# Kernel tuning notes

Measured on AMD Instinct MI355X. Metric: run time of the kernel, lower is better.

## Reference

```python
import jax, jax.numpy as jnp
import numpy as np

HEAD_NUM = 16
MASK_FILL = 100000.0  # source uses +1e5 on masked entries (not -inf)


def setup_inputs() -> dict:
    key = jax.random.key(0)
    k1, k2, k3, k4, k5 = jax.random.split(key, 5)
    B, S, E = 2, 2048, 1024
    scale = 0.02
    return {
        "x": jax.random.normal(k1, (B, S, E), dtype=jnp.float32),
        "W_atten": jax.random.normal(k2, (E, 3 * E), dtype=jnp.float32) * scale,
        "b_atten": jax.random.normal(k3, (3 * E,), dtype=jnp.float32) * scale,
        "W_proj": jax.random.normal(k4, (E, E), dtype=jnp.float32) * scale,
        "b_proj": jax.random.normal(k5, (E,), dtype=jnp.float32) * scale,
    }


def reference(x, W_atten, b_atten, W_proj, b_proj):
    B, S, E = x.shape
    H = HEAD_NUM
    hd = E // H
    # QKV projection: [B, S, 3E]
    qkv = x @ W_atten + b_atten
    # reshape [B, S, H, 3*hd] -> [B, H, S, 3*hd], chunk into q,k,v [B,H,S,hd]
    qkv = jnp.transpose(qkv.reshape(B, S, H, 3 * hd), (0, 2, 1, 3))
    q, k, v = jnp.split(qkv, 3, axis=-1)
    # raw scores, NO 1/sqrt(dk) scaling (faithful to source)
    w = jnp.einsum("bhqd,bhkd->bhqk", q, k)
    # causal mask applied as w*mask + (1-mask)*1e5 (faithful to source)
    mask = jnp.tril(jnp.ones((S, S), dtype=w.dtype))
    w = w * mask + (1.0 - mask) * MASK_FILL
    # softmax over dim=1 == HEAD axis (faithful to source quirk)
    w = jax.nn.softmax(w, axis=1)
    # attn_drop: identity in eval mode
    a = jnp.einsum("bhqk,bhkd->bhqd", w, v)  # [B,H,S,hd]
    a = jnp.transpose(a, (0, 2, 1, 3)).reshape(B, S, E)
    h = a @ W_proj + b_proj
    # resi_drop: identity in eval mode
    return h
```

## Files before the change

kernel.cpp:

```cpp
#include <hip/hip_runtime.h>

#define DI __device__ __forceinline__

typedef __attribute__((ext_vector_type(8))) short s16x8;
typedef __attribute__((ext_vector_type(4))) short s16x4;
typedef __attribute__((ext_vector_type(4))) float f32x4;

DI unsigned short f2bf(float f){
  unsigned u = __float_as_uint(f);
  u = (u + 0x7FFFu + ((u >> 16) & 1u)) >> 16;
  return (unsigned short)u;
}
DI float bf2f(unsigned short h){
  return __uint_as_float(((unsigned)h) << 16);
}

DI void gll16(const void* g, void* l){
  __builtin_amdgcn_global_load_lds((const __attribute__((address_space(1))) void*)g,
                                   (__attribute__((address_space(3))) void*)l, 16, 0, 0);
}

__global__ void cvt_kernel(const float* __restrict__ in, unsigned short* __restrict__ out, int n8){
  int i = blockIdx.x * blockDim.x + threadIdx.x;
  if (i >= n8) return;
  const float4* p = (const float4*)in + (size_t)i * 2;
  float4 a = p[0], b = p[1];
  s16x8 o;
  o[0] = (short)f2bf(a.x); o[1] = (short)f2bf(a.y); o[2] = (short)f2bf(a.z); o[3] = (short)f2bf(a.w);
  o[4] = (short)f2bf(b.x); o[5] = (short)f2bf(b.y); o[6] = (short)f2bf(b.z); o[7] = (short)f2bf(b.w);
  ((s16x8*)out)[i] = o;
}

__global__ void transpose_cvt(const float* __restrict__ in, unsigned short* __restrict__ out, int R, int C){
  __shared__ float t[32][33];
  int c0 = blockIdx.x * 32, r0 = blockIdx.y * 32;
  int tx = threadIdx.x, ty = threadIdx.y;
  #pragma unroll
  for (int i = 0; i < 4; i++)
    t[ty + i*8][tx] = in[(size_t)(r0 + ty + i*8) * C + c0 + tx];
  __syncthreads();
  #pragma unroll
  for (int i = 0; i < 4; i++)
    out[(size_t)(c0 + ty + i*8) * R + r0 + tx] = f2bf(t[tx][ty + i*8]);
}

template<int MODE, int BM>
__launch_bounds__(256)
__global__ void gemm_kernel(const unsigned short* __restrict__ A,
                            const unsigned short* __restrict__ Wt,
                            const float* __restrict__ bias,
                            int N,
                            unsigned short* __restrict__ qb,
                            unsigned short* __restrict__ kb,
                            unsigned short* __restrict__ vt,
                            float* __restrict__ out)
{
  constexpr int MI = BM / 32;
  constexpr int AC = BM / 32;
  const int K = 1024;
  __shared__ unsigned short As[BM * 64];
  __shared__ unsigned short Bs[128 * 64];
  int m0 = blockIdx.y * BM, n0 = blockIdx.x * 128;
  int tid = threadIdx.x;
  int lane = tid & 63, w = tid >> 6;
  int row_l = lane & 15, kgrp = lane >> 4;
  int wm = (w >> 1) * (MI * 16), wn = (w & 1) * 64;

  const unsigned short* asrc[AC];
  const unsigned short* bsrc[4];
  int ldsoA[AC], ldsoB[4];
  int chunk = (lane & 7) ^ (lane >> 3);
  #pragma unroll
  for (int c4 = 0; c4 < AC; c4++){
    int r = c4*32 + w*8 + (lane >> 3);
    asrc[c4] = A + (size_t)(m0 + r) * K + chunk*8;
    ldsoA[c4] = (c4*32 + w*8) * 64;
  }
  #pragma unroll
  for (int c4 = 0; c4 < 4; c4++){
    int r = c4*32 + w*8 + (lane >> 3);
    bsrc[c4] = Wt + (size_t)(n0 + r) * K + chunk*8;
    ldsoB[c4] = (c4*32 + w*8) * 64;
  }
  int eA[MI], eB[4];
  #pragma unroll
  for (int i = 0; i < MI; i++){
    int ra = wm + i*16 + row_l;
    eA[i] = (ra*64 + kgrp*8) ^ ((ra & 7) << 3);
  }
  #pragma unroll
  for (int i = 0; i < 4; i++){
    int rb = wn + i*16 + row_l;
    eB[i] = (rb*64 + kgrp*8) ^ ((rb & 7) << 3);
  }

  f32x4 acc[MI][4];
  #pragma unroll
  for (int i = 0; i < MI; i++)
    #pragma unroll
    for (int j = 0; j < 4; j++)
      acc[i][j] = (f32x4){0.f, 0.f, 0.f, 0.f};

  for (int k0 = 0; k0 < K; k0 += 64){
    #pragma unroll
    for (int c4 = 0; c4 < AC; c4++)
      gll16(asrc[c4] + k0, (void*)(As + ldsoA[c4]));
    #pragma unroll
    for (int c4 = 0; c4 < 4; c4++)
      gll16(bsrc[c4] + k0, (void*)(Bs + ldsoB[c4]));
    __syncthreads();
    #pragma unroll
    for (int kc = 0; kc < 2; kc++){
      s16x8 af[MI], bfr[4];
      #pragma unroll
      for (int mi = 0; mi < MI; mi++)
        af[mi] = *(const s16x8*)&As[eA[mi] ^ (kc*32)];
      #pragma unroll
      for (int ni = 0; ni < 4; ni++)
        bfr[ni] = *(const s16x8*)&Bs[eB[ni] ^ (kc*32)];
      #pragma unroll
      for (int mi = 0; mi < MI; mi++)
        #pragma unroll
        for (int ni = 0; ni < 4; ni++)
          acc[mi][ni] = __builtin_amdgcn_mfma_f32_16x16x32_bf16(af[mi], bfr[ni], acc[mi][ni], 0, 0, 0);
    }
    __syncthreads();
  }

  #pragma unroll
  for (int mi = 0; mi < MI; mi++){
    #pragma unroll
    for (int ni = 0; ni < 4; ni++){
      #pragma unroll
      for (int j = 0; j < 4; j++){
        int gr = m0 + wm + mi*16 + kgrp*4 + j;
        int gc = n0 + wn + ni*16 + row_l;
        float v = acc[mi][ni][j] + bias[gc];
        if (MODE == 0){
          int h = gc / 192, cc = gc % 192;
          int b = gr >> 11, s = gr & 2047;
          unsigned short bv = f2bf(v);
          if (cc < 64){
            qb[(size_t)gr * 1024 + h*64 + cc] = bv;
          } else if (cc < 128){
            int d = cc - 64; int kt = s >> 6, kk = s & 63;
            kb[(size_t)((b*16 + h)*32 + kt) * 4096 + ((kk*64 + d) ^ ((kk & 7) << 3))] = bv;
          } else {
            int d = cc - 128; int kt = s >> 6, kk = s & 63;
            vt[(size_t)((b*16 + h)*32 + kt) * 4096 + ((d*64 + kk) ^ ((d & 7) << 3))] = bv;
          }
        } else {
          out[(size_t)gr * N + gc] = v;
        }
      }
    }
  }
}

__global__ void sufv_kernel(const unsigned short* __restrict__ vt, float* __restrict__ sufv){
  __shared__ float tot[4][64];
  int bh = blockIdx.x;
  int tid = threadIdx.x;
  int tq = tid >> 6, d = tid & 63;
  const unsigned short* base = vt + (size_t)bh * 32 * 4096;
  float s[8];
  float run = 0.f;
  for (int j = 7; j >= 0; j--){
    int t = tq*8 + j;
    float rs = 0.f;
    #pragma unroll
    for (int c = 0; c < 8; c++){
      int idx = (d*64 + c*8) ^ ((d & 7) << 3);
      s16x8 v = *(const s16x8*)&base[(size_t)t*4096 + idx];
      #pragma unroll
      for (int e = 0; e < 8; e++) rs += bf2f((unsigned short)v[e]);
    }
    run += rs; s[j] = run;
  }
  tot[tq][d] = run;
  __syncthreads();
  float carry = 0.f;
  for (int t2 = tq+1; t2 < 4; t2++) carry += tot[t2][d];
  #pragma unroll
  for (int j = 0; j < 8; j++)
    sufv[((size_t)bh*33 + tq*8 + j)*64 + d] = s[j] + carry;
  if (tid < 64) sufv[((size_t)bh*33 + 32)*64 + tid] = 0.f;
}

__launch_bounds__(256)
__global__ void dpass_kernel(const unsigned short* __restrict__ qbuf,
                             const unsigned short* __restrict__ kb,
                             float* __restrict__ invDQ)
{
  __shared__ unsigned short Kst[4][4096];
  int bid = blockIdx.x;
  int blk = (bid & 7) * 132 + (bid >> 3);
  int b = blk / 528, t = blk % 528;
  int kt = (int)(32.5f - sqrtf(1056.25f - 2.f*t));
  while (kt*(65-kt)/2 > t) kt--;
  while ((kt+1)*(64-kt)/2 <= t) kt++;
  int qt = kt + (t - kt*(65-kt)/2);

  int tid = threadIdx.x, lane = tid & 63, w = tid >> 6;
  int row_l = lane & 15, kgrp = lane >> 4;

  const unsigned short* ktb = kb + ((size_t)(b*16)*32 + kt) * 4096;
  int sgoff = (w*128 + lane)*8;

  auto stage = [&](int hh, int buf){
    const unsigned short* src = ktb + (size_t)hh * 131072;
    gll16(src + sgoff,       (void*)(&Kst[buf][0] + w*1024));
    gll16(src + sgoff + 512, (void*)(&Kst[buf][0] + w*1024 + 512));
  };

  int e0[4];
  #pragma unroll
  for (int ks = 0; ks < 4; ks++){
    int row = ks*16 + row_l;
    e0[ks] = (row*64 + kgrp*8) ^ ((row & 7) << 3);
  }

  stage(0, 0);
  stage(1, 1);

  f32x4 esum[4];
  #pragma unroll
  for (int ks = 0; ks < 4; ks++) esum[ks] = (f32x4){0.f,0.f,0.f,0.f};

  const unsigned short* qrow_p = qbuf + (size_t)(b*2048 + qt*64 + w*16 + row_l) * 1024;
  s16x8 qf0 = *(const s16x8*)&qrow_p[kgrp*8];
  s16x8 qf1 = *(const s16x8*)&qrow_p[32 + kgrp*8];

  for (int h = 0; h < 16; h++){
    s16x8 qn0, qn1;
    if (h < 15){
      qn0 = *(const s16x8*)&qrow_p[(h+1)*64 + kgrp*8];
      qn1 = *(const s16x8*)&qrow_p[(h+1)*64 + 32 + kgrp*8];
    }
    if (h + 2 < 16) stage(h+2, (h+2) & 3);
    __builtin_amdgcn_sched_barrier(0);
    if (h < 14)      asm volatile("s_waitcnt vmcnt(8)" ::: "memory");
    else if (h < 15) asm volatile("s_waitcnt vmcnt(6)" ::: "memory");
    else             asm volatile("s_waitcnt vmcnt(2)" ::: "memory");
    __builtin_amdgcn_sched_barrier(0);
    __builtin_amdgcn_s_barrier();
    __builtin_amdgcn_sched_barrier(0);

    const unsigned short* kl = &Kst[h & 3][0];
    #pragma unroll
    for (int ks = 0; ks < 4; ks++){
      s16x8 a0 = *(const s16x8*)&kl[e0[ks]];
      s16x8 a1 = *(const s16x8*)&kl[e0[ks] ^ 32];
      f32x4 sc = __builtin_amdgcn_mfma_f32_16x16x32_bf16(a0, qf0, (f32x4){0.f,0.f,0.f,0.f}, 0, 0, 0);
      sc = __builtin_amdgcn_mfma_f32_16x16x32_bf16(a1, qf1, sc, 0, 0, 0);
      #pragma unroll
      for (int j = 0; j < 4; j++) esum[ks][j] += __expf(sc[j]);
    }
    if (h < 15){ qf0 = qn0; qf1 = qn1; }
  }

  int qcol = qt*64 + w*16 + row_l;
  float* dst = invDQ + (size_t)b*4194304 + (size_t)qcol*2048 + kt*64 + kgrp*4;
  #pragma unroll
  for (int ks = 0; ks < 4; ks++){
    f32x4 rv;
    #pragma unroll
    for (int j = 0; j < 4; j++) rv[j] = 1.f / esum[ks][j];
    *(f32x4*)&dst[ks*16] = rv;
  }
}

__launch_bounds__(256)
__global__ void pv_kernel(const unsigned short* __restrict__ qbuf,
                          const unsigned short* __restrict__ kb,
                          const unsigned short* __restrict__ vt,
                          const float* __restrict__ invDQ,
                          const float* __restrict__ sufv,
                          unsigned short* __restrict__ ab,
                          float* __restrict__ pb)
{
  __shared__ unsigned short Kst[2][4096];
  __shared__ unsigned short Vst[2][4096];
  __shared__ unsigned short Wsh[4][1152];

  int blk = ((blockIdx.x & 7) << 7) + (blockIdx.x >> 3);
  int b = blk >> 9;
  int r = blk & 511;
  int h = r >> 5;
  int r2 = r & 31;
  int i = r2 >> 1, half = r2 & 1;
  int qsm = i, qbig = 31 - i;

  int tid = threadIdx.x, lane = tid & 63, w = tid >> 6;
  int row_l = lane & 15, kgrp = lane >> 4;

  const unsigned short* KT = kb + (size_t)((b*16 + h)*32) * 4096;
  const unsigned short* VT = vt + (size_t)((b*16 + h)*32) * 4096;
  int sgoff = (w*128 + lane)*8;
  unsigned short* Wsw = &Wsh[w][0];

  int eK[4];
  #pragma unroll
  for (int ks = 0; ks < 4; ks++){
    int row = ks*16 + row_l;
    eK[ks] = (row*64 + kgrp*8) ^ ((row & 7) << 3);
  }

  auto stage = [&](int kt, int buf){
    gll16(KT + (size_t)kt*4096 + sgoff,       (void*)(&Kst[buf][0] + w*1024));
    gll16(KT + (size_t)kt*4096 + sgoff + 512, (void*)(&Kst[buf][0] + w*1024 + 512));
    gll16(VT + (size_t)kt*4096 + sgoff,       (void*)(&Vst[buf][0] + w*1024));
    gll16(VT + (size_t)kt*4096 + sgoff + 512, (void*)(&Vst[buf][0] + w*1024 + 512));
  };

  auto run = [&](int qt, int k0t, int k1t, int mode){
    int q0 = qt * 64;
    int qv = q0 + w*16 + row_l;
    const unsigned short* qrow_p = qbuf + (size_t)(b*2048 + qv) * 1024 + h*64;
    s16x8 qf0 = *(const s16x8*)&qrow_p[kgrp*8];
    s16x8 qf1 = *(const s16x8*)&qrow_p[32 + kgrp*8];
    const float* ivrow = invDQ + (size_t)b*4194304 + (size_t)qv*2048 + kgrp*4;

    f32x4 pvv[4];
    #pragma unroll
    for (int d = 0; d < 4; d++) pvv[d] = (f32x4){0.f,0.f,0.f,0.f};

    __syncthreads();
    stage(k0t, 0);
    f32x4 inxt[4];
    #pragma unroll
    for (int ks = 0; ks < 4; ks++) inxt[ks] = *(const f32x4*)&ivrow[k0t*64 + ks*16];

    for (int kt = k0t; kt < k1t; kt++){
      int bufc = (kt - k0t) & 1;
      bool nx = (kt + 1 < k1t);
      __builtin_amdgcn_s_barrier();
      if (nx) stage(kt+1, bufc ^ 1);
      f32x4 icur[4];
      #pragma unroll
      for (int ks = 0; ks < 4; ks++) icur[ks] = inxt[ks];
      if (nx){
        #pragma unroll
        for (int ks = 0; ks < 4; ks++) inxt[ks] = *(const f32x4*)&ivrow[(kt+1)*64 + ks*16];
      }
      __builtin_amdgcn_sched_barrier(0);
      if (nx) asm volatile("s_waitcnt vmcnt(12)" ::: "memory");
      else    asm volatile("s_waitcnt vmcnt(4)" ::: "memory");
      __builtin_amdgcn_sched_barrier(0);
      __builtin_amdgcn_s_barrier();
      __builtin_amdgcn_sched_barrier(0);

      const unsigned short* kl = &Kst[bufc][0];
      const unsigned short* vl = &Vst[bufc][0];
      f32x4 sc[4];
      #pragma unroll
      for (int ks = 0; ks < 4; ks++){
        s16x8 a0 = *(const s16x8*)&kl[eK[ks]];
        s16x8 a1 = *(const s16x8*)&kl[eK[ks] ^ 32];
        sc[ks] = __builtin_amdgcn_mfma_f32_16x16x32_bf16(a0, qf0, (f32x4){0.f,0.f,0.f,0.f}, 0, 0, 0);
        sc[ks] = __builtin_amdgcn_mfma_f32_16x16x32_bf16(a1, qf1, sc[ks], 0, 0, 0);
      }
      int kbase = kt*64 + kgrp*4;
      #pragma unroll
      for (int ks = 0; ks < 4; ks++){
        #pragma unroll
        for (int j = 0; j < 4; j++){
          float e = __expf(sc[ks][j]);
          sc[ks][j] = (kbase + ks*16 + j > qv) ? 0.0625f : e * icur[ks][j];
        }
        unsigned lo, hi;
        asm("v_cvt_pk_bf16_f32 %0, %1, %2" : "=v"(lo) : "v"(sc[ks][0]), "v"(sc[ks][1]));
        asm("v_cvt_pk_bf16_f32 %0, %1, %2" : "=v"(hi) : "v"(sc[ks][2]), "v"(sc[ks][3]));
        uint2 pk2; pk2.x = lo; pk2.y = hi;
        *(uint2*)&Wsw[row_l*72 + ks*16 + kgrp*4] = pk2;
      }
      #pragma unroll
      for (int kc = 0; kc < 2; kc++){
        s16x8 af = *(const s16x8*)&Wsw[row_l*72 + kc*32 + kgrp*8];
        #pragma unroll
        for (int dq = 0; dq < 4; dq++){
          s16x8 vf = *(const s16x8*)&vl[eK[dq] ^ (kc*32)];
          pvv[dq] = __builtin_amdgcn_mfma_f32_16x16x32_bf16(af, vf, pvv[dq], 0, 0, 0);
        }
      }
    }

    if (mode == 0){
      int tsuf = qt + 1;
      #pragma unroll
      for (int dq = 0; dq < 4; dq++){
        int d = dq*16 + row_l;
        float suf = sufv[((size_t)(b*16 + h)*33 + tsuf)*64 + d];
        #pragma unroll
        for (int j = 0; j < 4; j++){
          int qo = q0 + w*16 + kgrp*4 + j;
          ab[(size_t)(b*2048 + qo)*1024 + h*64 + d] = f2bf(pvv[dq][j] + 0.0625f * suf);
        }
      }
    } else {
      float* pr = pb + ((size_t)((b*16 + h)*16 + i)*2 + (mode - 1)) * 4096;
      #pragma unroll
      for (int dq = 0; dq < 4; dq++){
        int d = dq*16 + row_l;
        #pragma unroll
        for (int j = 0; j < 4; j++)
          pr[(w*16 + kgrp*4 + j)*64 + d] = pvv[dq][j];
      }
    }
  };

  if (half == 0){
    run(qsm, 0, i + 1, 0);
    run(qbig, 0, 16 - i, 1);
  } else {
    run(qbig, 16 - i, 32 - i, 2);
  }
}

__global__ void reduce_kernel(const float* __restrict__ pb,
                              const float* __restrict__ sufv,
                              unsigned short* __restrict__ ab)
{
  int blk = blockIdx.x;
  int b = blk >> 8, rr = blk & 255;
  int h = rr >> 4, i = rr & 15;
  int qbig = 31 - i, tsuf = 32 - i;
  int t = threadIdx.x;
  int q = t >> 2, dbase = (t & 3) * 16;
  const float* p0 = pb + ((size_t)((b*16 + h)*16 + i)*2 + 0)*4096 + q*64 + dbase;
  const float* p1 = p0 + 4096;
  const float* sf = sufv + ((size_t)(b*16 + h)*33 + tsuf)*64 + dbase;
  unsigned short* op = ab + (size_t)(b*2048 + qbig*64 + q)*1024 + h*64 + dbase;
  #pragma unroll
  for (int e = 0; e < 4; e++){
    float4 a = *(const float4*)(p0 + e*4);
    float4 bb = *(const float4*)(p1 + e*4);
    float4 s = *(const float4*)(sf + e*4);
    unsigned short o[4];
    o[0] = f2bf(a.x + bb.x + 0.0625f * s.x);
    o[1] = f2bf(a.y + bb.y + 0.0625f * s.y);
    o[2] = f2bf(a.z + bb.z + 0.0625f * s.z);
    o[3] = f2bf(a.w + bb.w + 0.0625f * s.w);
    *(s16x4*)(op + e*4) = *(s16x4*)o;
  }
}

extern "C" void kernel_launch(void* const* d_in, const int* in_sizes, int n_in,
                              void* d_out, int out_size, void* d_ws, size_t ws_size,
                              hipStream_t stream) {
  (void)in_sizes; (void)n_in; (void)out_size; (void)ws_size;
  const float* x  = (const float*)d_in[0];
  const float* Wa = (const float*)d_in[1];
  const float* ba = (const float*)d_in[2];
  const float* Wp = (const float*)d_in[3];
  const float* bp = (const float*)d_in[4];
  float* out = (float*)d_out;

  char* ws = (char*)d_ws;
  size_t off = 0;
  auto alloc = [&](size_t bytes) -> void* {
    void* p = ws + off;
    off += (bytes + 255) & ~(size_t)255;
    return p;
  };
  float* pbuf          = (float*)alloc((size_t)16*1024*1024);
  unsigned short* xb   = (unsigned short*)((char*)pbuf);
  unsigned short* WaT  = (unsigned short*)((char*)pbuf + (size_t)4096*1024*2);
  unsigned short* WpT  = (unsigned short*)alloc((size_t)1024*1024*2);
  unsigned short* qbuf = (unsigned short*)alloc((size_t)4096*1024*2);
  unsigned short* ktile= (unsigned short*)alloc((size_t)4096*1024*2);
  unsigned short* vtile= (unsigned short*)alloc((size_t)4096*1024*2);
  unsigned short* abuf = (unsigned short*)alloc((size_t)4096*1024*2);
  float* invDQ         = (float*)alloc((size_t)2*2048*2048*4);
  float* sufv          = (float*)alloc((size_t)32*33*64*4);

  cvt_kernel<<<2048, 256, 0, stream>>>(x, xb, 4096*1024/8);
  transpose_cvt<<<dim3(3072/32, 1024/32), dim3(32, 8), 0, stream>>>(Wa, WaT, 1024, 3072);
  transpose_cvt<<<dim3(1024/32, 1024/32), dim3(32, 8), 0, stream>>>(Wp, WpT, 1024, 1024);

  gemm_kernel<0,128><<<dim3(24, 32), 256, 0, stream>>>(xb, WaT, ba, 3072, qbuf, ktile, vtile, nullptr);

  sufv_kernel<<<32, 256, 0, stream>>>(vtile, sufv);

  dpass_kernel<<<1056, 256, 0, stream>>>(qbuf, ktile, invDQ);

  pv_kernel<<<1024, 256, 0, stream>>>(qbuf, ktile, vtile, invDQ, sufv, abuf, pbuf);

  reduce_kernel<<<512, 256, 0, stream>>>(pbuf, sufv, abuf);

  gemm_kernel<1,64><<<dim3(1024/128, 4096/64), 256, 0, stream>>>(abuf, WpT, bp, 1024, nullptr, nullptr, nullptr, out);
}
```

Baseline: 182.8 us.

## Split pv_kernel into single-wave blocks loading K/V tiles straight into registers

Restructures pv_kernel so each 64-thread block handles one wave's 16 query rows, and launches 4x as many blocks. The K and V tiles now go straight from global memory into registers with software prefetch, replacing the shared-memory double buffer and its block-wide barriers. This removes LDS staging and synchronisation cost. In exchange, each wave reads K/V from global/L2 on its own, which quadruples the K/V traffic, and register pressure rises. The swizzled address pattern is kept in global reads, so the loads are less contiguous per lane.

```diff
diff --git a/kernel.cpp b/kernel.cpp
--- a/kernel.cpp
+++ b/kernel.cpp
@@ -270,7 +270,7 @@
   }
 }
 
-__launch_bounds__(256)
+__launch_bounds__(64, 4)
 __global__ void pv_kernel(const unsigned short* __restrict__ qbuf,
                           const unsigned short* __restrict__ kb,
                           const unsigned short* __restrict__ vt,
@@ -279,39 +279,27 @@
                           unsigned short* __restrict__ ab,
                           float* __restrict__ pb)
 {
-  __shared__ unsigned short Kst[2][4096];
-  __shared__ unsigned short Vst[2][4096];
-  __shared__ unsigned short Wsh[4][1152];
-
-  int blk = ((blockIdx.x & 7) << 7) + (blockIdx.x >> 3);
-  int b = blk >> 9;
-  int r = blk & 511;
-  int h = r >> 5;
-  int r2 = r & 31;
-  int i = r2 >> 1, half = r2 & 1;
+  __shared__ unsigned short Wsw[16 * 72];
+
+  int bid = blockIdx.x;
+  int blk = ((bid & 7) << 9) | (bid >> 3);
+  int w    = blk & 3;
+  int half = (blk >> 2) & 1;
+  int i    = (blk >> 3) & 15;
+  int h    = (blk >> 7) & 15;
+  int b    = blk >> 11;
   int qsm = i, qbig = 31 - i;
 
-  int tid = threadIdx.x, lane = tid & 63, w = tid >> 6;
+  int lane = threadIdx.x & 63;
   int row_l = lane & 15, kgrp = lane >> 4;
 
   const unsigned short* KT = kb + (size_t)((b*16 + h)*32) * 4096;
   const unsigned short* VT = vt + (size_t)((b*16 + h)*32) * 4096;
-  int sgoff = (w*128 + lane)*8;
-  unsigned short* Wsw = &Wsh[w][0];
 
   int eK[4];
   #pragma unroll
-  for (int ks = 0; ks < 4; ks++){
-    int row = ks*16 + row_l;
-    eK[ks] = (row*64 + kgrp*8) ^ ((row & 7) << 3);
-  }
-
-  auto stage = [&](int kt, int buf){
-    gll16(KT + (size_t)kt*4096 + sgoff,       (void*)(&Kst[buf][0] + w*1024));
-    gll16(KT + (size_t)kt*4096 + sgoff + 512, (void*)(&Kst[buf][0] + w*1024 + 512));
-    gll16(VT + (size_t)kt*4096 + sgoff,       (void*)(&Vst[buf][0] + w*1024));
-    gll16(VT + (size_t)kt*4096 + sgoff + 512, (void*)(&Vst[buf][0] + w*1024 + 512));
-  };
+  for (int ks = 0; ks < 4; ks++)
+    eK[ks] = ((ks*16 + row_l)*64 + kgrp*8) ^ ((row_l & 7) << 3);
 
   auto run = [&](int qt, int k0t, int k1t, int mode){
     int q0 = qt * 64;
@@ -325,52 +313,46 @@
     #pragma unroll
     for (int d = 0; d < 4; d++) pvv[d] = (f32x4){0.f,0.f,0.f,0.f};
 
-    __syncthreads();
-    stage(k0t, 0);
-    f32x4 inxt[4];
-    #pragma unroll
-    for (int ks = 0; ks < 4; ks++) inxt[ks] = *(const f32x4*)&ivrow[k0t*64 + ks*16];
+    const unsigned short* kp = KT + (size_t)k0t*4096;
+    const unsigned short* vp = VT + (size_t)k0t*4096;
+    s16x8 kr[8], vr[8];
+    #pragma unroll
+    for (int ks = 0; ks < 4; ks++){
+      kr[2*ks]   = *(const s16x8*)&kp[eK[ks]];
+      kr[2*ks+1] = *(const s16x8*)&kp[eK[ks] ^ 32];
+    }
+    #pragma unroll
+    for (int kc = 0; kc < 2; kc++)
+      #pragma unroll
+      for (int dq = 0; dq < 4; dq++)
+        vr[kc*4+dq] = *(const s16x8*)&vp[eK[dq] ^ (kc*32)];
 
     for (int kt = k0t; kt < k1t; kt++){
-      int bufc = (kt - k0t) & 1;
       bool nx = (kt + 1 < k1t);
-      __builtin_amdgcn_s_barrier();
-      if (nx) stage(kt+1, bufc ^ 1);
-      f32x4 icur[4];
-      #pragma unroll
-      for (int ks = 0; ks < 4; ks++) icur[ks] = inxt[ks];
-      if (nx){
-        #pragma unroll
-        for (int ks = 0; ks < 4; ks++) inxt[ks] = *(const f32x4*)&ivrow[(kt+1)*64 + ks*16];
-      }
-      __builtin_amdgcn_sched_barrier(0);
-      if (nx) asm volatile("s_waitcnt vmcnt(12)" ::: "memory");
-      else    asm volatile("s_waitcnt vmcnt(4)" ::: "memory");
-      __builtin_amdgcn_sched_barrier(0);
-      __builtin_amdgcn_s_barrier();
-      __builtin_amdgcn_sched_barrier(0);
-
-      const unsigned short* kl = &Kst[bufc][0];
-      const unsigned short* vl = &Vst[bufc][0];
-      f32x4 sc[4];
+      const unsigned short* kn = KT + (size_t)(kt+1)*4096;
+      const unsigned short* vn = VT + (size_t)(kt+1)*4096;
+      f32x4 iv[4];
+      #pragma unroll
+      for (int ks = 0; ks < 4; ks++)
+        iv[ks] = *(const f32x4*)&ivrow[kt*64 + ks*16];
+
+      int kbase = kt*64 + kgrp*4;
       #pragma unroll
       for (int ks = 0; ks < 4; ks++){
-        s16x8 a0 = *(const s16x8*)&kl[eK[ks]];
-        s16x8 a1 = *(const s16x8*)&kl[eK[ks] ^ 32];
-        sc[ks] = __builtin_amdgcn_mfma_f32_16x16x32_bf16(a0, qf0, (f32x4){0.f,0.f,0.f,0.f}, 0, 0, 0);
-        sc[ks] = __builtin_amdgcn_mfma_f32_16x16x32_bf16(a1, qf1, sc[ks], 0, 0, 0);
-      }
-      int kbase = kt*64 + kgrp*4;
-      #pragma unroll
-      for (int ks = 0; ks < 4; ks++){
+        f32x4 sc = __builtin_amdgcn_mfma_f32_16x16x32_bf16(kr[2*ks], qf0, (f32x4){0.f,0.f,0.f,0.f}, 0, 0, 0);
+        sc = __builtin_amdgcn_mfma_f32_16x16x32_bf16(kr[2*ks+1], qf1, sc, 0, 0, 0);
+        if (nx){
+          kr[2*ks]   = *(const s16x8*)&kn[eK[ks]];
+          kr[2*ks+1] = *(const s16x8*)&kn[eK[ks] ^ 32];
+        }
         #pragma unroll
         for (int j = 0; j < 4; j++){
-          float e = __expf(sc[ks][j]);
-          sc[ks][j] = (kbase + ks*16 + j > qv) ? 0.0625f : e * icur[ks][j];
+          float e = __expf(sc[j]);
+          sc[j] = (kbase + ks*16 + j > qv) ? 0.0625f : e * iv[ks][j];
         }
         unsigned lo, hi;
-        asm("v_cvt_pk_bf16_f32 %0, %1, %2" : "=v"(lo) : "v"(sc[ks][0]), "v"(sc[ks][1]));
-        asm("v_cvt_pk_bf16_f32 %0, %1, %2" : "=v"(hi) : "v"(sc[ks][2]), "v"(sc[ks][3]));
+        asm("v_cvt_pk_bf16_f32 %0, %1, %2" : "=v"(lo) : "v"(sc[0]), "v"(sc[1]));
+        asm("v_cvt_pk_bf16_f32 %0, %1, %2" : "=v"(hi) : "v"(sc[2]), "v"(sc[3]));
         uint2 pk2; pk2.x = lo; pk2.y = hi;
         *(uint2*)&Wsw[row_l*72 + ks*16 + kgrp*4] = pk2;
       }
@@ -378,10 +360,15 @@
       for (int kc = 0; kc < 2; kc++){
         s16x8 af = *(const s16x8*)&Wsw[row_l*72 + kc*32 + kgrp*8];
         #pragma unroll
-        for (int dq = 0; dq < 4; dq++){
-          s16x8 vf = *(const s16x8*)&vl[eK[dq] ^ (kc*32)];
-          pvv[dq] = __builtin_amdgcn_mfma_f32_16x16x32_bf16(af, vf, pvv[dq], 0, 0, 0);
-        }
+        for (int dq = 0; dq < 4; dq++)
+          pvv[dq] = __builtin_amdgcn_mfma_f32_16x16x32_bf16(af, vr[kc*4+dq], pvv[dq], 0, 0, 0);
+      }
+      if (nx){
+        #pragma unroll
+        for (int kc = 0; kc < 2; kc++)
+          #pragma unroll
+          for (int dq = 0; dq < 4; dq++)
+            vr[kc*4+dq] = *(const s16x8*)&vn[eK[dq] ^ (kc*32)];
       }
     }
 
@@ -484,7 +471,7 @@
 
   dpass_kernel<<<1056, 256, 0, stream>>>(qbuf, ktile, invDQ);
 
-  pv_kernel<<<1024, 256, 0, stream>>>(qbuf, ktile, vtile, invDQ, sufv, abuf, pbuf);
+  pv_kernel<<<4096, 64, 0, stream>>>(qbuf, ktile, vtile, invDQ, sufv, abuf, pbuf);
 
   reduce_kernel<<<512, 256, 0, stream>>>(pbuf, sufv, abuf);
 
```

Measured after the change: 273.7 us. 49.8% more time.
